# Optimization experiments

Measured on AMD Instinct MI355X. Metric: run time of the kernel, lower is better.

## Reference

```python
import jax, jax.numpy as jnp
import numpy as np

H = 128  # hidden_size hard-coded in AttentionSeqModel


def setup_inputs() -> dict:
    key = jax.random.key(0)
    ks = jax.random.split(key, 20)
    B, L, D, A = 512, 512, 128, 16  # batch, num_light, obs_size, action_size

    def p(k, shape, s=0.05):
        return jax.random.normal(k, shape, dtype=jnp.float32) * s

    return {
        "obs": jax.random.normal(ks[0], (B, L, D), dtype=jnp.float32),
        # encoder params
        "enc_emb_W": p(ks[1], (H, D)), "enc_emb_b": p(ks[2], (H,)),
        "enc_Wih": p(ks[3], (3 * H, H)), "enc_Whh": p(ks[4], (3 * H, H)),
        "enc_bih": p(ks[5], (3 * H,)), "enc_bhh": p(ks[6], (3 * H,)),
        # decoder params
        "dec_emb_W": p(ks[7], (H, A)), "dec_emb_b": p(ks[8], (H,)),
        "attn_W": p(ks[9], (L, 2 * H)), "attn_b": p(ks[10], (L,)),
        "comb_W": p(ks[11], (H, 2 * H)), "comb_b": p(ks[12], (H,)),
        "dec_Wih": p(ks[13], (3 * H, H)), "dec_Whh": p(ks[14], (3 * H, H)),
        "dec_bih": p(ks[15], (3 * H,)), "dec_bhh": p(ks[16], (3 * H,)),
        "out_W": p(ks[17], (A, H)), "out_b": p(ks[18], (A,)),
    }


def _gru_cell(x, h, Wih, Whh, bih, bhh):
    # torch.nn.GRU single-step semantics
    gi = x @ Wih.T + bih          # (B, 3H)
    gh = h @ Whh.T + bhh          # (B, 3H)
    ir, iz, inn = jnp.split(gi, 3, axis=-1)
    hr, hz, hn = jnp.split(gh, 3, axis=-1)
    r = jax.nn.sigmoid(ir + hr)
    z = jax.nn.sigmoid(iz + hz)
    n = jnp.tanh(inn + r * hn)
    return (1.0 - z) * n + z * h


def reference(obs, enc_emb_W, enc_emb_b, enc_Wih, enc_Whh, enc_bih, enc_bhh,
              dec_emb_W, dec_emb_b, attn_W, attn_b, comb_W, comb_b,
              dec_Wih, dec_Whh, dec_bih, dec_bhh, out_W, out_b):
    B, L, _ = obs.shape
    A = out_b.shape[0]

    # ---- encoder loop over num_light timesteps ----
    def enc_step(h, x_t):
        emb = x_t @ enc_emb_W.T + enc_emb_b           # (B, H)
        h2 = _gru_cell(emb, h, enc_Wih, enc_Whh, enc_bih, enc_bhh)
        # original stores encoder_output[0, 0]: only batch element 0
        return h2, h2[0]

    h0 = jnp.zeros((B, H), obs.dtype)
    hN, enc_outs = jax.lax.scan(enc_step, h0, jnp.swapaxes(obs, 0, 1))
    # enc_outs: (L, H)

    # ---- decoder loop, feeding log-softmax logits back as input ----
    def dec_step(carry, _):
        inp, h = carry
        emb = inp @ dec_emb_W.T + dec_emb_b           # (B, H); dropout = identity (eval)
        aw = jax.nn.softmax(jnp.concatenate([emb, h], axis=1) @ attn_W.T + attn_b, axis=1)  # (B, L)
        applied = aw @ enc_outs                        # (B, H)
        o = jax.nn.relu(jnp.concatenate([emb, applied], axis=1) @ comb_W.T + comb_b)
        h2 = _gru_cell(o, h, dec_Wih, dec_Whh, dec_bih, dec_bhh)
        logits = jax.nn.log_softmax(h2 @ out_W.T + out_b, axis=1)  # (B, A)
        return (logits, h2), None

    init = (jnp.zeros((B, A), obs.dtype), hN)
    (logits, _), _ = jax.lax.scan(dec_step, init, None, length=L)
    return logits
```

## Files before the change

kernel.cpp:

```cpp
#include <hip/hip_runtime.h>
#include <stdint.h>

#define H_  128
#define L_  512
#define B_  512
#define A_  16
#define G3_ 384

#define OFF_M1    0
#define OFF_WHHE  98304
#define OFF_WB    196608
#define OFF_WIH   327680
#define OFF_WHH   425984
#define OFF_WC2   524288
#define OFF_PA    557056
#define OFF_PC    573440
#define OFF_OUTW  577536
#define OFF_BGI   581632
#define OFF_ZB    583168
#define OFF_OB    585216
#define OFF_ENC   585728
#define OFF_HN    716800

typedef _Float16 f16_t;
typedef __attribute__((ext_vector_type(2))) _Float16 f16x2_t;

__device__ __forceinline__ float dot2f(uint32_t w, uint32_t a, float acc) {
#if __has_builtin(__builtin_amdgcn_fdot2)
  return __builtin_amdgcn_fdot2(__builtin_bit_cast(f16x2_t, w),
                                __builtin_bit_cast(f16x2_t, a), acc, false);
#else
  f16x2_t x = __builtin_bit_cast(f16x2_t, w);
  f16x2_t y = __builtin_bit_cast(f16x2_t, a);
  return acc + (float)x.x * (float)y.x + (float)x.y * (float)y.y;
#endif
}

__device__ __forceinline__ uint32_t pk2(float lo, float hi) {
#if __has_builtin(__builtin_amdgcn_cvt_pkrtz)
  return __builtin_bit_cast(uint32_t, __builtin_amdgcn_cvt_pkrtz(lo, hi));
#else
  f16x2_t v; v.x = (_Float16)lo; v.y = (_Float16)hi;
  return __builtin_bit_cast(uint32_t, v);
#endif
}

__device__ __forceinline__ float sigm(float x) { return 1.f / (1.f + __expf(-x)); }
__device__ __forceinline__ float tanh_s(float t) { float ex = __expf(2.f * t); return 1.f - 2.f / (ex + 1.f); }
__device__ __forceinline__ float gru1(float ir, float iz, float in_, float hr, float hz, float hn, float h) {
  float rg = sigm(ir + hr);
  float zg = sigm(iz + hz);
  float nn = tanh_s(in_ + rg * hn);
  return (1.f - zg) * nn + zg * h;
}

#define LDS4(arr, idx) (*(const uint4*)&(arr)[(idx)])

__global__ void prep_kernel(const float* __restrict__ enc_emb_W, const float* __restrict__ enc_emb_b,
                            const float* __restrict__ enc_Wih, const float* __restrict__ enc_bih,
                            const float* __restrict__ dec_emb_W, const float* __restrict__ dec_emb_b,
                            const float* __restrict__ attn_W, const float* __restrict__ attn_b,
                            const float* __restrict__ comb_W, const float* __restrict__ comb_b,
                            const float* __restrict__ dec_Wih, const float* __restrict__ dec_Whh,
                            const float* __restrict__ enc_Whh, const float* __restrict__ out_W,
                            char* __restrict__ ws) {
  int t = blockIdx.x * 256 + threadIdx.x;
  if (t < 49152) {
    int n = t >> 7, d = t & 127; float acc = 0.f;
    for (int h = 0; h < 128; ++h) acc += enc_Wih[n*128+h] * enc_emb_W[h*128+d];
    ((f16_t*)(ws+OFF_M1))[t] = (f16_t)acc; return;
  } t -= 49152;
  if (t < 384) {
    float acc = enc_bih[t];
    for (int h = 0; h < 128; ++h) acc += enc_Wih[t*128+h] * enc_emb_b[h];
    ((float*)(ws+OFF_BGI))[t] = acc; return;
  } t -= 384;
  if (t < 8192) {
    int l = t >> 4, a = t & 15; float acc = 0.f;
    for (int k = 0; k < 128; ++k) acc += attn_W[l*256+k] * dec_emb_W[k*16+a];
    ((f16_t*)(ws+OFF_PA))[t] = (f16_t)acc; return;
  } t -= 8192;
  if (t < 512) {
    float acc = attn_b[t];
    for (int k = 0; k < 128; ++k) acc += attn_W[t*256+k] * dec_emb_b[k];
    ((float*)(ws+OFF_ZB))[t] = acc; return;
  } t -= 512;
  if (t < 2048) {
    int j = t >> 4, a = t & 15; float acc = 0.f;
    for (int k = 0; k < 128; ++k) acc += comb_W[j*256+k] * dec_emb_W[k*16+a];
    ((f16_t*)(ws+OFF_PC))[t] = (f16_t)acc; return;
  } t -= 2048;
  if (t < 128) {
    float acc = comb_b[t];
    for (int k = 0; k < 128; ++k) acc += comb_W[t*256+k] * dec_emb_b[k];
    ((float*)(ws+OFF_OB))[t] = acc; return;
  } t -= 128;
  if (t < 65536) {
    int l = t >> 7, k = t & 127;
    ((f16_t*)(ws+OFF_WB))[t] = (f16_t)attn_W[l*256+128+k]; return;
  } t -= 65536;
  if (t < 49152) { ((f16_t*)(ws+OFF_WHHE))[t] = (f16_t)enc_Whh[t]; return; } t -= 49152;
  if (t < 49152) { ((f16_t*)(ws+OFF_WIH))[t]  = (f16_t)dec_Wih[t]; return; } t -= 49152;
  if (t < 49152) { ((f16_t*)(ws+OFF_WHH))[t]  = (f16_t)dec_Whh[t]; return; } t -= 49152;
  if (t < 16384) {
    int j = t >> 7, k = t & 127;
    ((f16_t*)(ws+OFF_WC2))[t] = (f16_t)comb_W[j*256+128+k]; return;
  } t -= 16384;
  if (t < 2048) { ((f16_t*)(ws+OFF_OUTW))[t] = (f16_t)out_W[t]; return; }
}

__global__ __launch_bounds__(512, 1) void enc_kernel(const float* __restrict__ obs,
                                                     const float* __restrict__ enc_bhh,
                                                     char* __restrict__ ws) {
  __shared__ __align__(16) uint32_t obspk[2][64];
  __shared__ __align__(16) uint32_t hpk[2][64];
  __shared__ __align__(16) float    gi_s[2][G3_];
  __shared__ __align__(16) float    gh_s[2][G3_];
  __shared__ float bgi_s[G3_], bhh_s[G3_];

  const int tid = threadIdx.x, bid = blockIdx.x;
  const uint32_t* M1u  = (const uint32_t*)(ws + OFF_M1);
  const uint32_t* WHu  = (const uint32_t*)(ws + OFF_WHHE);
  const float*    bgi  = (const float*)(ws + OFF_BGI);
  f16_t* encw = (f16_t*)(ws + OFF_ENC);
  float* hN   = (float*)(ws + OFF_HN);

  uint32_t m1r[64], whr[64];
  if (tid < G3_) {
    const uint4* p1 = (const uint4*)(M1u + tid*64);
    const uint4* p2 = (const uint4*)(WHu + tid*64);
#pragma unroll
    for (int q = 0; q < 16; ++q) {
      uint4 v = p1[q]; m1r[q*4]=v.x; m1r[q*4+1]=v.y; m1r[q*4+2]=v.z; m1r[q*4+3]=v.w;
      uint4 w = p2[q]; whr[q*4]=w.x; whr[q*4+1]=w.y; whr[q*4+2]=w.z; whr[q*4+3]=w.w;
    }
    bgi_s[tid] = bgi[tid]; bhh_s[tid] = enc_bhh[tid];
  }

  const int r = tid >> 7, jj = tid & 127;
  const size_t rowbase = (size_t)(2*bid + r) * L_ * H_ + jj;
  float hreg = 0.f;
  float oA = 0.f;
  if (tid < 256) {
    float o0 = obs[rowbase + 0*H_];
    float op = __shfl_xor(o0, 1);
    if (!(jj & 1)) obspk[r][jj >> 1] = pk2(o0, op);
    oA = obs[rowbase + 1*H_];
  }
  if (tid < 128) hpk[tid>>6][tid&63] = 0u;
  __syncthreads();

#pragma unroll 1
  for (int t = 0; t < L_; ++t) {
    float oB = 0.f;
    if (tid < 256) {
      int tn = (t+2 < L_) ? t+2 : L_-1;
      oB = obs[rowbase + (size_t)tn*H_];
    }
    if (tid < G3_) {
      float g0 = bgi_s[tid], g1 = g0, ga = 0.f, gb = 0.f;
      float e0 = bhh_s[tid], e1 = e0, ea = 0.f, eb = 0.f;
#pragma unroll
      for (int c = 0; c < 16; ++c) {
        uint4 o0 = LDS4(obspk[0], c*4); uint4 o1 = LDS4(obspk[1], c*4);
        uint4 h0 = LDS4(hpk[0],  c*4);  uint4 h1 = LDS4(hpk[1],  c*4);
        g0 = dot2f(m1r[c*4+0], o0.x, g0); g0 = dot2f(m1r[c*4+1], o0.y, g0);
        ga = dot2f(m1r[c*4+2], o0.z, ga); ga = dot2f(m1r[c*4+3], o0.w, ga);
        g1 = dot2f(m1r[c*4+0], o1.x, g1); g1 = dot2f(m1r[c*4+1], o1.y, g1);
        gb = dot2f(m1r[c*4+2], o1.z, gb); gb = dot2f(m1r[c*4+3], o1.w, gb);
        e0 = dot2f(whr[c*4+0], h0.x, e0); e0 = dot2f(whr[c*4+1], h0.y, e0);
        ea = dot2f(whr[c*4+2], h0.z, ea); ea = dot2f(whr[c*4+3], h0.w, ea);
        e1 = dot2f(whr[c*4+0], h1.x, e1); e1 = dot2f(whr[c*4+1], h1.y, e1);
        eb = dot2f(whr[c*4+2], h1.z, eb); eb = dot2f(whr[c*4+3], h1.w, eb);
      }
      gi_s[0][tid] = g0+ga; gi_s[1][tid] = g1+gb;
      gh_s[0][tid] = e0+ea; gh_s[1][tid] = e1+eb;
    }
    __syncthreads();
    if (tid < 256) {
      float ir = gi_s[r][jj], iz = gi_s[r][jj+128], in_ = gi_s[r][jj+256];
      float hr = gh_s[r][jj], hz = gh_s[r][jj+128], hn = gh_s[r][jj+256];
      float h2 = gru1(ir, iz, in_, hr, hz, hn, hreg);
      hreg = h2;
      float hp = __shfl_xor(h2, 1);
      float op = __shfl_xor(oA, 1);
      if (!(jj & 1)) {
        hpk[r][jj >> 1] = pk2(h2, hp);
        obspk[r][jj >> 1] = pk2(oA, op);
      }
      if (bid == 0 && r == 0) encw[t*H_ + jj] = (f16_t)h2;
      oA = oB;
    }
    __syncthreads();
  }
  if (tid < 256) hN[(2*bid + r)*H_ + jj] = hreg;
}

__global__ __launch_bounds__(512, 1) void dec_kernel(const float* __restrict__ dec_bih,
                                                     const float* __restrict__ dec_bhh,
                                                     const float* __restrict__ out_b,
                                                     char* __restrict__ ws,
                                                     float* __restrict__ dout) {
  __shared__ __align__(16) uint32_t encI[32768];
  __shared__ __align__(16) uint32_t owL[1024];
  __shared__ __align__(16) uint32_t awpk[2][272];
  __shared__ __align__(16) uint32_t aplpk[2][64];
  __shared__ __align__(16) uint32_t gip[G3_];
  __shared__ __align__(16) uint32_t ghp[G3_];
  __shared__ __align__(16) uint32_t opk[2][64];
  __shared__ __align__(16) uint32_t hpk[2][64];
  __shared__ __align__(16) uint32_t inppk[2][8];
  __shared__ float reds[2][8];

  const int tid = threadIdx.x, bid = blockIdx.x;
  const uint32_t* WBu  = (const uint32_t*)(ws + OFF_WB);
  const uint32_t* WIu  = (const uint32_t*)(ws + OFF_WIH);
  const uint32_t* WHu  = (const uint32_t*)(ws + OFF_WHH);
  const uint32_t* WCu  = (const uint32_t*)(ws + OFF_WC2);
  const uint32_t* PAu  = (const uint32_t*)(ws + OFF_PA);
  const uint32_t* PCu  = (const uint32_t*)(ws + OFF_PC);
  const uint32_t* OWu  = (const uint32_t*)(ws + OFF_OUTW);
  const float*    zb   = (const float*)(ws + OFF_ZB);
  const float*    obg  = (const float*)(ws + OFF_OB);
  const float*    hN   = (const float*)(ws + OFF_HN);

  uint32_t wb[64], wA[64], wB[64];
  {
    const uint4* p = (const uint4*)(WBu + tid*64);
#pragma unroll
    for (int q = 0; q < 16; ++q) { uint4 v = p[q]; wb[q*4]=v.x; wb[q*4+1]=v.y; wb[q*4+2]=v.z; wb[q*4+3]=v.w; }
  }
  if (tid < G3_) {
    const uint4* p = (const uint4*)(WIu + tid*64);
    const uint4* p2 = (const uint4*)(WHu + tid*64);
#pragma unroll
    for (int q = 0; q < 16; ++q) {
      uint4 v = p[q];  wA[q*4]=v.x; wA[q*4+1]=v.y; wA[q*4+2]=v.z; wA[q*4+3]=v.w;
      uint4 w = p2[q]; wB[q*4]=w.x; wB[q*4+1]=w.y; wB[q*4+2]=w.z; wB[q*4+3]=w.w;
    }
  } else {
    const uint4* p = (const uint4*)(WCu + (tid-384)*64);
#pragma unroll
    for (int q = 0; q < 16; ++q) {
      uint4 v = p[q]; wA[q*4]=v.x; wA[q*4+1]=v.y; wA[q*4+2]=v.z; wA[q*4+3]=v.w;
    }
  }
  uint32_t paq[8], pcq[8];
  {
    uint4 v0 = *(const uint4*)(PAu + tid*8);
    uint4 v1 = *(const uint4*)(PAu + tid*8 + 4);
    paq[0]=v0.x; paq[1]=v0.y; paq[2]=v0.z; paq[3]=v0.w;
    paq[4]=v1.x; paq[5]=v1.y; paq[6]=v1.z; paq[7]=v1.w;
  }
  if (tid >= G3_) {
    uint4 v0 = *(const uint4*)(PCu + (tid-G3_)*8);
    uint4 v1 = *(const uint4*)(PCu + (tid-G3_)*8 + 4);
    pcq[0]=v0.x; pcq[1]=v0.y; pcq[2]=v0.z; pcq[3]=v0.w;
    pcq[4]=v1.x; pcq[5]=v1.y; pcq[6]=v1.z; pcq[7]=v1.w;
  } else {
#pragma unroll
    for (int q = 0; q < 8; ++q) pcq[q] = 0u;
  }

  {
    int k = tid & 127, ls = tid >> 7;
    const uint16_t* eg = (const uint16_t*)(ws + OFF_ENC);
    uint16_t* ei = (uint16_t*)encI;
    for (int cc = 0; cc < 16; ++cc) {
      int c = ls*16 + cc;
#pragma unroll
      for (int p = 0; p < 8; ++p) ei[(c*128 + k)*8 + p] = eg[(c*8 + p)*128 + k];
    }
  }
  for (int idx = tid; idx < 1024; idx += 512) {
    int qq = idx & 3, rest = idx >> 2, a = rest & 15, c = rest >> 4;
    owL[(c*16 + a)*4 + qq] = OWu[a*64 + c*4 + qq];
  }
  const float zbias    = zb[tid];
  const float bih_reg  = (tid < G3_) ? dec_bih[tid] : 0.f;
  const float bhh_reg  = (tid < G3_) ? dec_bhh[tid] : 0.f;
  const float ob_reg   = (tid >= G3_) ? obg[tid - G3_] : 0.f;
  const float outb_reg = (tid < 128) ? out_b[tid & 15] : 0.f;
  if (tid < 16) inppk[tid>>3][tid&7] = 0u;

  float hA = 0.f, hB = 0.f;
  if (tid < 128) {
    int w = tid >> 6, lane = tid & 63;
    hA = hN[(2*bid + w)*H_ + 2*lane];
    hB = hN[(2*bid + w)*H_ + 2*lane + 1];
    hpk[w][lane] = pk2(hA, hB);
  }
  __syncthreads();

#pragma unroll 1
  for (int t = 0; t < L_; ++t) {
    {
      uint4 i0 = LDS4(inppk[0], 0), i0b = LDS4(inppk[0], 4);
      uint4 i1 = LDS4(inppk[1], 0), i1b = LDS4(inppk[1], 4);
      float a0 = dot2f(paq[0], i0.x, zbias); a0 = dot2f(paq[1], i0.y, a0);
      a0 = dot2f(paq[2], i0.z, a0);          a0 = dot2f(paq[3], i0.w, a0);
      float b0 = dot2f(paq[4], i0b.x, 0.f);  b0 = dot2f(paq[5], i0b.y, b0);
      b0 = dot2f(paq[6], i0b.z, b0);         b0 = dot2f(paq[7], i0b.w, b0);
      float a1 = dot2f(paq[0], i1.x, zbias); a1 = dot2f(paq[1], i1.y, a1);
      a1 = dot2f(paq[2], i1.z, a1);          a1 = dot2f(paq[3], i1.w, a1);
      float b1 = dot2f(paq[4], i1b.x, 0.f);  b1 = dot2f(paq[5], i1b.y, b1);
      b1 = dot2f(paq[6], i1b.z, b1);         b1 = dot2f(paq[7], i1b.w, b1);
#pragma unroll
      for (int c = 0; c < 16; ++c) {
        uint4 h0 = LDS4(hpk[0], c*4); uint4 h1 = LDS4(hpk[1], c*4);
        a0 = dot2f(wb[c*4+0], h0.x, a0); a0 = dot2f(wb[c*4+1], h0.y, a0);
        b0 = dot2f(wb[c*4+2], h0.z, b0); b0 = dot2f(wb[c*4+3], h0.w, b0);
        a1 = dot2f(wb[c*4+0], h1.x, a1); a1 = dot2f(wb[c*4+1], h1.y, a1);
        b1 = dot2f(wb[c*4+2], h1.z, b1); b1 = dot2f(wb[c*4+3], h1.w, b1);
      }
      float e0 = __expf(a0 + b0), e1 = __expf(a1 + b1);
      float s0 = e0, s1 = e1;
#pragma unroll
      for (int off = 32; off; off >>= 1) { s0 += __shfl_xor(s0, off); s1 += __shfl_xor(s1, off); }
      int wv = tid >> 6;
      if ((tid & 63) == 0) { reds[0][wv] = s0; reds[1][wv] = s1; }
      float ep0 = __shfl_xor(e0, 1), ep1 = __shfl_xor(e1, 1);
      int awi = (tid >> 1) + ((tid >> 7) << 2);
      if (!(tid & 1)) { awpk[0][awi] = pk2(e0, ep0); awpk[1][awi] = pk2(e1, ep1); }
    }
    __syncthreads();
    {
      int lane = tid & 63, wv3 = tid >> 6;
      int k = wv3*16 + (lane & 15), chunk = lane >> 4;
      float S0 = 0.f, S1 = 0.f;
#pragma unroll
      for (int i = 0; i < 8; ++i) { S0 += reds[0][i]; S1 += reds[1][i]; }
      float is0 = 1.f / S0, is1 = 1.f / S1;
      int eb0 = chunk*8192 + k*4;
      int awb = chunk*68;
      float a00=0.f, a01=0.f, a10=0.f, a11=0.f;
#pragma unroll
      for (int cc = 0; cc < 8; ++cc) {
        uint4 ev = *(const uint4*)&encI[eb0 + cc*512];
        uint4 w0 = *(const uint4*)&awpk[0][awb + cc*4];
        uint4 wq = *(const uint4*)&awpk[1][awb + cc*4];
        a00 = dot2f(ev.x, w0.x, a00); a00 = dot2f(ev.y, w0.y, a00);
        a00 = dot2f(ev.z, w0.z, a00); a00 = dot2f(ev.w, w0.w, a00);
        a10 = dot2f(ev.x, wq.x, a10); a10 = dot2f(ev.y, wq.y, a10);
        a10 = dot2f(ev.z, wq.z, a10); a10 = dot2f(ev.w, wq.w, a10);
      }
#pragma unroll
      for (int cc = 8; cc < 16; ++cc) {
        uint4 ev = *(const uint4*)&encI[eb0 + cc*512];
        uint4 w0 = *(const uint4*)&awpk[0][awb + cc*4];
        uint4 wq = *(const uint4*)&awpk[1][awb + cc*4];
        a01 = dot2f(ev.x, w0.x, a01); a01 = dot2f(ev.y, w0.y, a01);
        a01 = dot2f(ev.z, w0.z, a01); a01 = dot2f(ev.w, w0.w, a01);
        a11 = dot2f(ev.x, wq.x, a11); a11 = dot2f(ev.y, wq.y, a11);
        a11 = dot2f(ev.z, wq.z, a11); a11 = dot2f(ev.w, wq.w, a11);
      }
      float v0 = (a00 + a01) * is0;
      float v1 = (a10 + a11) * is1;
      v0 += __shfl_xor(v0, 16); v0 += __shfl_xor(v0, 32);
      v1 += __shfl_xor(v1, 16); v1 += __shfl_xor(v1, 32);
      float v0p = __shfl_xor(v0, 1), v1p = __shfl_xor(v1, 1);
      if (!(lane & 49)) {
        int kk = k >> 1;
        aplpk[0][kk] = pk2(v0, v0p); aplpk[1][kk] = pk2(v1, v1p);
      }
    }
    __syncthreads();
    if (tid >= G3_) {
      int jj = tid - G3_;
      uint4 i0 = LDS4(inppk[0], 0), i0b = LDS4(inppk[0], 4);
      uint4 i1 = LDS4(inppk[1], 0), i1b = LDS4(inppk[1], 4);
      float o0 = dot2f(pcq[0], i0.x, ob_reg); o0 = dot2f(pcq[1], i0.y, o0);
      o0 = dot2f(pcq[2], i0.z, o0);           o0 = dot2f(pcq[3], i0.w, o0);
      float oa = dot2f(pcq[4], i0b.x, 0.f);   oa = dot2f(pcq[5], i0b.y, oa);
      oa = dot2f(pcq[6], i0b.z, oa);          oa = dot2f(pcq[7], i0b.w, oa);
      float o1 = dot2f(pcq[0], i1.x, ob_reg); o1 = dot2f(pcq[1], i1.y, o1);
      o1 = dot2f(pcq[2], i1.z, o1);           o1 = dot2f(pcq[3], i1.w, o1);
      float obb = dot2f(pcq[4], i1b.x, 0.f);  obb = dot2f(pcq[5], i1b.y, obb);
      obb = dot2f(pcq[6], i1b.z, obb);        obb = dot2f(pcq[7], i1b.w, obb);
#pragma unroll
      for (int c = 0; c < 16; ++c) {
        uint4 p0 = LDS4(aplpk[0], c*4); uint4 p1 = LDS4(aplpk[1], c*4);
        o0 = dot2f(wA[c*4+0], p0.x, o0); o0 = dot2f(wA[c*4+1], p0.y, o0);
        oa = dot2f(wA[c*4+2], p0.z, oa); oa = dot2f(wA[c*4+3], p0.w, oa);
        o1 = dot2f(wA[c*4+0], p1.x, o1); o1 = dot2f(wA[c*4+1], p1.y, o1);
        obb = dot2f(wA[c*4+2], p1.z, obb); obb = dot2f(wA[c*4+3], p1.w, obb);
      }
      o0 = fmaxf(o0 + oa, 0.f); o1 = fmaxf(o1 + obb, 0.f);
      float px0 = __shfl_xor(o0, 1), px1 = __shfl_xor(o1, 1);
      if (!(jj & 1)) { opk[0][jj>>1] = pk2(o0, px0); opk[1][jj>>1] = pk2(o1, px1); }
    } else {
      float e0g = bhh_reg, e1g = e0g, ea = 0.f, eb = 0.f;
#pragma unroll
      for (int c = 0; c < 16; ++c) {
        uint4 h0 = LDS4(hpk[0], c*4); uint4 h1 = LDS4(hpk[1], c*4);
        e0g = dot2f(wB[c*4+0], h0.x, e0g); e0g = dot2f(wB[c*4+1], h0.y, e0g);
        ea  = dot2f(wB[c*4+2], h0.z, ea);  ea  = dot2f(wB[c*4+3], h0.w, ea);
        e1g = dot2f(wB[c*4+0], h1.x, e1g); e1g = dot2f(wB[c*4+1], h1.y, e1g);
        eb  = dot2f(wB[c*4+2], h1.z, eb);  eb  = dot2f(wB[c*4+3], h1.w, eb);
      }
      ghp[tid] = pk2(e0g + ea, e1g + eb);
    }
    __syncthreads();
    if (tid < G3_) {
      float g0 = bih_reg, g1 = g0, ga = 0.f, gb = 0.f;
#pragma unroll
      for (int c = 0; c < 16; ++c) {
        uint4 o0 = LDS4(opk[0], c*4); uint4 o1 = LDS4(opk[1], c*4);
        g0 = dot2f(wA[c*4+0], o0.x, g0); g0 = dot2f(wA[c*4+1], o0.y, g0);
        ga = dot2f(wA[c*4+2], o0.z, ga); ga = dot2f(wA[c*4+3], o0.w, ga);
        g1 = dot2f(wA[c*4+0], o1.x, g1); g1 = dot2f(wA[c*4+1], o1.y, g1);
        gb = dot2f(wA[c*4+2], o1.z, gb); gb = dot2f(wA[c*4+3], o1.w, gb);
      }
      gip[tid] = pk2(g0 + ga, g1 + gb);
    }
    __syncthreads();
    if (tid < 128) {
      int w = tid >> 6, lane = tid & 63;
      uint2 gA = *(const uint2*)&gip[2*lane];
      uint2 gB = *(const uint2*)&gip[128 + 2*lane];
      uint2 gC = *(const uint2*)&gip[256 + 2*lane];
      uint2 eA = *(const uint2*)&ghp[2*lane];
      uint2 eB = *(const uint2*)&ghp[128 + 2*lane];
      uint2 eC = *(const uint2*)&ghp[256 + 2*lane];
#define SEL(u) (w ? (float)(__builtin_bit_cast(f16x2_t,(u)).y) : (float)(__builtin_bit_cast(f16x2_t,(u)).x))
      hA = gru1(SEL(gA.x), SEL(gB.x), SEL(gC.x), SEL(eA.x), SEL(eB.x), SEL(eC.x), hA);
      hB = gru1(SEL(gA.y), SEL(gB.y), SEL(gC.y), SEL(eA.y), SEL(eB.y), SEL(eC.y), hB);
#undef SEL
      hpk[w][lane] = pk2(hA, hB);
      asm volatile("s_waitcnt lgkmcnt(0)" ::: "memory");
      int a = lane & 15, kh = lane >> 4;
      float y = (kh == 0) ? outb_reg : 0.f;
#pragma unroll
      for (int cc = 0; cc < 4; ++cc) {
        int c = kh*4 + cc;
        uint4 ww = *(const uint4*)&owL[(c*16 + a)*4];
        uint4 hb = LDS4(hpk[w], c*4);
        y = dot2f(ww.x, hb.x, y); y = dot2f(ww.y, hb.y, y);
        y = dot2f(ww.z, hb.z, y); y = dot2f(ww.w, hb.w, y);
      }
      y += __shfl_xor(y, 16); y += __shfl_xor(y, 32);
      if (lane < 16) {
        float e = __expf(y);
        float s = e;
#pragma unroll
        for (int off = 8; off; off >>= 1) s += __shfl_xor(s, off);
        float lsf = y - __logf(s);
        if (t == L_-1) dout[(2*bid + w)*A_ + a] = lsf;
        float pr = __shfl_xor(lsf, 1);
        if (!(a & 1)) inppk[w][a >> 1] = pk2(lsf, pr);
      }
    }
    __syncthreads();
  }
}

extern "C" void kernel_launch(void* const* d_in, const int* in_sizes, int n_in,
                              void* d_out, int out_size, void* d_ws, size_t ws_size,
                              hipStream_t stream) {
  (void)in_sizes; (void)n_in; (void)out_size; (void)ws_size;
  const float* obs       = (const float*)d_in[0];
  const float* enc_emb_W = (const float*)d_in[1];
  const float* enc_emb_b = (const float*)d_in[2];
  const float* enc_Wih   = (const float*)d_in[3];
  const float* enc_Whh   = (const float*)d_in[4];
  const float* enc_bih   = (const float*)d_in[5];
  const float* enc_bhh   = (const float*)d_in[6];
  const float* dec_emb_W = (const float*)d_in[7];
  const float* dec_emb_b = (const float*)d_in[8];
  const float* attn_W    = (const float*)d_in[9];
  const float* attn_b    = (const float*)d_in[10];
  const float* comb_W    = (const float*)d_in[11];
  const float* comb_b    = (const float*)d_in[12];
  const float* dec_Wih   = (const float*)d_in[13];
  const float* dec_Whh   = (const float*)d_in[14];
  const float* dec_bih   = (const float*)d_in[15];
  const float* dec_bhh   = (const float*)d_in[16];
  const float* out_W     = (const float*)d_in[17];
  const float* out_b     = (const float*)d_in[18];
  char* ws = (char*)d_ws;

  hipLaunchKernelGGL(prep_kernel, dim3(1140), dim3(256), 0, stream,
                     enc_emb_W, enc_emb_b, enc_Wih, enc_bih, dec_emb_W, dec_emb_b,
                     attn_W, attn_b, comb_W, comb_b, dec_Wih, dec_Whh, enc_Whh, out_W, ws);
  hipLaunchKernelGGL(enc_kernel, dim3(256), dim3(512), 0, stream, obs, enc_bhh, ws);
  hipLaunchKernelGGL(dec_kernel, dim3(256), dim3(512), 0, stream,
                     dec_bih, dec_bhh, out_b, ws, (float*)d_out);
}
```

Measured before the change: 3.754 ms.

## Restructure attention-apply as per-wave partial sums to drop a block barrier

Each wave now computes partial attention-weighted sums over its own 64 encoder positions straight from its exp values, written to a wave-private buffer. This needs only an intra-wave wait instead of a block barrier before the apply step. The last two waves then reduce the 8 partials, normalize, and pack the result into wave-private copies before the combine step, removing one __syncthreads per decoder step. The cost is extra LDS traffic for the partial reduction and reliance on intra-wave LDS ordering via s_waitcnt.

Result: slower. 4.525 ms (+20.6%).

```diff
diff --git a/kernel.cpp b/kernel.cpp
--- a/kernel.cpp
+++ b/kernel.cpp
@@ -203,8 +203,9 @@
                                                      float* __restrict__ dout) {
   __shared__ __align__(16) uint32_t encI[32768];
   __shared__ __align__(16) uint32_t owL[1024];
-  __shared__ __align__(16) uint32_t awpk[2][272];
-  __shared__ __align__(16) uint32_t aplpk[2][64];
+  __shared__ __align__(16) uint32_t ewv[8][2][36];
+  __shared__ __align__(16) float    aplred[8][2][128];
+  __shared__ __align__(16) uint32_t aplpkW[2][2][64];
   __shared__ __align__(16) uint32_t gip[G3_];
   __shared__ __align__(16) uint32_t ghp[G3_];
   __shared__ __align__(16) uint32_t opk[2][64];
@@ -295,6 +296,7 @@
 #pragma unroll 1
   for (int t = 0; t < L_; ++t) {
     {
+      const int wv = tid >> 6, lane = tid & 63;
       uint4 i0 = LDS4(inppk[0], 0), i0b = LDS4(inppk[0], 4);
       uint4 i1 = LDS4(inppk[1], 0), i1b = LDS4(inppk[1], 4);
       float a0 = dot2f(paq[0], i0.x, zbias); a0 = dot2f(paq[1], i0.y, a0);
@@ -317,55 +319,52 @@
       float s0 = e0, s1 = e1;
 #pragma unroll
       for (int off = 32; off; off >>= 1) { s0 += __shfl_xor(s0, off); s1 += __shfl_xor(s1, off); }
-      int wv = tid >> 6;
-      if ((tid & 63) == 0) { reds[0][wv] = s0; reds[1][wv] = s1; }
+      if (lane == 0) { reds[0][wv] = s0; reds[1][wv] = s1; }
       float ep0 = __shfl_xor(e0, 1), ep1 = __shfl_xor(e1, 1);
-      int awi = (tid >> 1) + ((tid >> 7) << 2);
-      if (!(tid & 1)) { awpk[0][awi] = pk2(e0, ep0); awpk[1][awi] = pk2(e1, ep1); }
-    }
-    __syncthreads();
-    {
-      int lane = tid & 63, wv3 = tid >> 6;
-      int k = wv3*16 + (lane & 15), chunk = lane >> 4;
+      if (!(lane & 1)) {
+        ewv[wv][0][lane >> 1] = pk2(e0, ep0);
+        ewv[wv][1][lane >> 1] = pk2(e1, ep1);
+      }
+      asm volatile("s_waitcnt lgkmcnt(0)" ::: "memory");
+      float p00 = 0.f, p01 = 0.f, p10 = 0.f, p11 = 0.f;
+#pragma unroll
+      for (int cc = 0; cc < 8; ++cc) {
+        int c = wv*8 + cc;
+        uint4 ev0 = LDS4(encI, (c*128 + lane)*4);
+        uint4 ev1 = LDS4(encI, (c*128 + lane + 64)*4);
+        uint4 ew0 = LDS4(ewv[wv][0], cc*4);
+        uint4 ew1 = LDS4(ewv[wv][1], cc*4);
+        p00 = dot2f(ev0.x, ew0.x, p00); p00 = dot2f(ev0.y, ew0.y, p00);
+        p00 = dot2f(ev0.z, ew0.z, p00); p00 = dot2f(ev0.w, ew0.w, p00);
+        p01 = dot2f(ev1.x, ew0.x, p01); p01 = dot2f(ev1.y, ew0.y, p01);
+        p01 = dot2f(ev1.z, ew0.z, p01); p01 = dot2f(ev1.w, ew0.w, p01);
+        p10 = dot2f(ev0.x, ew1.x, p10); p10 = dot2f(ev0.y, ew1.y, p10);
+        p10 = dot2f(ev0.z, ew1.z, p10); p10 = dot2f(ev0.w, ew1.w, p10);
+        p11 = dot2f(ev1.x, ew1.x, p11); p11 = dot2f(ev1.y, ew1.y, p11);
+        p11 = dot2f(ev1.z, ew1.z, p11); p11 = dot2f(ev1.w, ew1.w, p11);
+      }
+      aplred[wv][0][lane]      = p00;
+      aplred[wv][0][lane + 64] = p01;
+      aplred[wv][1][lane]      = p10;
+      aplred[wv][1][lane + 64] = p11;
+    }
+    __syncthreads();
+    if (tid >= G3_) {
+      const int l6 = tid & 63, ow = (tid >> 6) - 6;
       float S0 = 0.f, S1 = 0.f;
 #pragma unroll
       for (int i = 0; i < 8; ++i) { S0 += reds[0][i]; S1 += reds[1][i]; }
       float is0 = 1.f / S0, is1 = 1.f / S1;
-      int eb0 = chunk*8192 + k*4;
-      int awb = chunk*68;
-      float a00=0.f, a01=0.f, a10=0.f, a11=0.f;
-#pragma unroll
-      for (int cc = 0; cc < 8; ++cc) {
-        uint4 ev = *(const uint4*)&encI[eb0 + cc*512];
-        uint4 w0 = *(const uint4*)&awpk[0][awb + cc*4];
-        uint4 wq = *(const uint4*)&awpk[1][awb + cc*4];
-        a00 = dot2f(ev.x, w0.x, a00); a00 = dot2f(ev.y, w0.y, a00);
-        a00 = dot2f(ev.z, w0.z, a00); a00 = dot2f(ev.w, w0.w, a00);
-        a10 = dot2f(ev.x, wq.x, a10); a10 = dot2f(ev.y, wq.y, a10);
-        a10 = dot2f(ev.z, wq.z, a10); a10 = dot2f(ev.w, wq.w, a10);
-      }
-#pragma unroll
-      for (int cc = 8; cc < 16; ++cc) {
-        uint4 ev = *(const uint4*)&encI[eb0 + cc*512];
-        uint4 w0 = *(const uint4*)&awpk[0][awb + cc*4];
-        uint4 wq = *(const uint4*)&awpk[1][awb + cc*4];
-        a01 = dot2f(ev.x, w0.x, a01); a01 = dot2f(ev.y, w0.y, a01);
-        a01 = dot2f(ev.z, w0.z, a01); a01 = dot2f(ev.w, w0.w, a01);
-        a11 = dot2f(ev.x, wq.x, a11); a11 = dot2f(ev.y, wq.y, a11);
-        a11 = dot2f(ev.z, wq.z, a11); a11 = dot2f(ev.w, wq.w, a11);
-      }
-      float v0 = (a00 + a01) * is0;
-      float v1 = (a10 + a11) * is1;
-      v0 += __shfl_xor(v0, 16); v0 += __shfl_xor(v0, 32);
-      v1 += __shfl_xor(v1, 16); v1 += __shfl_xor(v1, 32);
-      float v0p = __shfl_xor(v0, 1), v1p = __shfl_xor(v1, 1);
-      if (!(lane & 49)) {
-        int kk = k >> 1;
-        aplpk[0][kk] = pk2(v0, v0p); aplpk[1][kk] = pk2(v1, v1p);
-      }
-    }
-    __syncthreads();
-    if (tid >= G3_) {
+      float a00 = 0.f, a01 = 0.f, a10 = 0.f, a11 = 0.f;
+#pragma unroll
+      for (int w = 0; w < 8; ++w) {
+        float2 v0 = *(const float2*)&aplred[w][0][2*l6];
+        float2 v1 = *(const float2*)&aplred[w][1][2*l6];
+        a00 += v0.x; a01 += v0.y; a10 += v1.x; a11 += v1.y;
+      }
+      aplpkW[ow][0][l6] = pk2(a00*is0, a01*is0);
+      aplpkW[ow][1][l6] = pk2(a10*is1, a11*is1);
+      asm volatile("s_waitcnt lgkmcnt(0)" ::: "memory");
       int jj = tid - G3_;
       uint4 i0 = LDS4(inppk[0], 0), i0b = LDS4(inppk[0], 4);
       uint4 i1 = LDS4(inppk[1], 0), i1b = LDS4(inppk[1], 4);
@@ -379,7 +378,7 @@
       obb = dot2f(pcq[6], i1b.z, obb);        obb = dot2f(pcq[7], i1b.w, obb);
 #pragma unroll
       for (int c = 0; c < 16; ++c) {
-        uint4 p0 = LDS4(aplpk[0], c*4); uint4 p1 = LDS4(aplpk[1], c*4);
+        uint4 p0 = LDS4(aplpkW[ow][0], c*4); uint4 p1 = LDS4(aplpkW[ow][1], c*4);
         o0 = dot2f(wA[c*4+0], p0.x, o0); o0 = dot2f(wA[c*4+1], p0.y, o0);
         oa = dot2f(wA[c*4+2], p0.z, oa); oa = dot2f(wA[c*4+3], p0.w, oa);
         o1 = dot2f(wA[c*4+0], p1.x, o1); o1 = dot2f(wA[c*4+1], p1.y, o1);
```
